# Kernel tuning notes

Measured on AMD Instinct MI355X. Metric: run time of the kernel, lower is better.

The kernel has to match this reference:

```python
import jax, jax.numpy as jnp
import numpy as np

B, S, I, Q, H = 512, 196, 2048, 1024, 512


def _attn(X, g, wx, bx, wg, bg, wh, bh):
    # X: (B, S, F); g: (B, G) or None
    feat = jnp.einsum('bsf,fh->bsh', X, wx) + bx
    if g is not None:
        feat = feat + (g @ wg + bg)[:, None, :]
    h = jnp.tanh(feat)
    score = jnp.einsum('bsh,h->bs', h, wh) + bh  # (B, S)
    a = jax.nn.softmax(score, axis=1)
    return jnp.einsum('bs,bsf->bf', a, X)


def setup_inputs() -> dict:
    key = jax.random.key(0)
    ks = jax.random.split(key, 16)
    sc = lambda n: 1.0 / np.sqrt(n)
    d = {
        'ques_feat': jax.random.normal(ks[0], (B, Q), jnp.float32),
        'img_feat': jax.random.normal(ks[1], (B, S, I), jnp.float32),
        # attn1: X=ques (Q), no guidance
        'w1x': jax.random.uniform(ks[2], (Q, H), jnp.float32, -sc(Q), sc(Q)),
        'b1x': jnp.zeros((H,), jnp.float32),
        'w1h': jax.random.uniform(ks[3], (H,), jnp.float32, -sc(H), sc(H)),
        'b1h': jnp.zeros((), jnp.float32),
        # attn2: X=img (I), guidance=ques (Q)
        'w2x': jax.random.uniform(ks[4], (I, H), jnp.float32, -sc(I), sc(I)),
        'b2x': jnp.zeros((H,), jnp.float32),
        'w2g': jax.random.uniform(ks[5], (Q, H), jnp.float32, -sc(Q), sc(Q)),
        'b2g': jnp.zeros((H,), jnp.float32),
        'w2h': jax.random.uniform(ks[6], (H,), jnp.float32, -sc(H), sc(H)),
        'b2h': jnp.zeros((), jnp.float32),
        # attn3: X=ques (Q), guidance=img-attended (I)
        'w3x': jax.random.uniform(ks[7], (Q, H), jnp.float32, -sc(Q), sc(Q)),
        'b3x': jnp.zeros((H,), jnp.float32),
        'w3g': jax.random.uniform(ks[8], (I, H), jnp.float32, -sc(I), sc(I)),
        'b3g': jnp.zeros((H,), jnp.float32),
        'w3h': jax.random.uniform(ks[9], (H,), jnp.float32, -sc(H), sc(H)),
        'b3h': jnp.zeros((), jnp.float32),
    }
    return d


def reference(ques_feat, img_feat, w1x, b1x, w1h, b1h, w2x, b2x, w2g, b2g,
              w2h, b2h, w3x, b3x, w3g, b3g, w3h, b3h):
    q = ques_feat[:, None, :]  # (B, 1, Q)
    ques_self = _attn(q, None, w1x, b1x, None, None, w1h, b1h)          # (B, Q)
    img_attn = _attn(img_feat, ques_self, w2x, b2x, w2g, b2g, w2h, b2h)  # (B, I)
    ques_attn = _attn(q, img_attn, w3x, b3x, w3g, b3g, w3h, b3h)         # (B, Q)
    return (ques_attn, img_attn)
```

## Files before the change

### kernel.cpp

```cpp
#include <hip/hip_runtime.h>
#include <hip/hip_bf16.h>
#include <cstdint>


typedef __attribute__((ext_vector_type(8))) short bf16x8;
typedef __attribute__((ext_vector_type(4))) float f32x4;

__device__ inline unsigned short f2bf(float f) {
    union { float f; unsigned u; } v; v.f = f;
    unsigned u = v.u;
    u += 0x7FFFu + ((u >> 16) & 1u);
    return (unsigned short)(u >> 16);
}

__device__ inline unsigned pk2(float lo, float hi) {
    __hip_bfloat162 h = __float22bfloat162_rn(make_float2(lo, hi));
    return *reinterpret_cast<unsigned*>(&h);
}

__global__ void k_copy(const float* __restrict__ src, float* __restrict__ dst) {
    int i = blockIdx.x * blockDim.x + threadIdx.x;
    reinterpret_cast<float4*>(dst)[i] = reinterpret_cast<const float4*>(src)[i];
}

__global__ void k_pack_w(const float* __restrict__ w, unsigned short* __restrict__ wtf) {
    int kblk = blockIdx.x >> 5;
    int nblk = blockIdx.x & 31;
    int t = threadIdx.x;
    int kc8 = t >> 4, col = t & 15;
    const float* src = w + (size_t)(kblk * 64 + kc8 * 8) * 512 + nblk * 16 + col;
    unsigned short* dst = wtf + (size_t)(kblk * 32 + nblk) * 1024 + kc8 * 128 + col * 8;
    unsigned short tmp[8];
    #pragma unroll
    for (int j = 0; j < 8; ++j) tmp[j] = f2bf(src[(size_t)j * 512]);
    *reinterpret_cast<uint4*>(dst) = *reinterpret_cast<const uint4*>(tmp);
}

__global__ void k_cconst(const float* __restrict__ qf, const float* __restrict__ w2g,
                         const float* __restrict__ b2g, const float* __restrict__ b2x,
                         float* __restrict__ cc) {
    __shared__ float qls[2][1024];
    int b0 = blockIdx.x * 2;
    int t = threadIdx.x;
    #pragma unroll
    for (int j = 0; j < 2; ++j) {
        int idx = j * 256 + t;
        int bb = idx >> 8, c4 = idx & 255;
        float4 v = reinterpret_cast<const float4*>(qf + (size_t)(b0 + bb) * 1024)[c4];
        qls[bb][c4 * 4 + 0] = v.x; qls[bb][c4 * 4 + 1] = v.y;
        qls[bb][c4 * 4 + 2] = v.z; qls[bb][c4 * 4 + 3] = v.w;
    }
    __syncthreads();
    float a00 = 0.f, a01 = 0.f, a10 = 0.f, a11 = 0.f;
    #pragma unroll 8
    for (int q = 0; q < 1024; ++q) {
        float w0 = w2g[q * 512 + t];
        float w1 = w2g[q * 512 + 256 + t];
        float q0 = qls[0][q], q1 = qls[1][q];
        a00 += q0 * w0; a01 += q0 * w1;
        a10 += q1 * w0; a11 += q1 * w1;
    }
    float c0 = b2g[t] + b2x[t];
    float c1 = b2g[t + 256] + b2x[t + 256];
    cc[(size_t)b0 * 512 + t] = a00 + c0;
    cc[(size_t)b0 * 512 + t + 256] = a01 + c1;
    cc[(size_t)(b0 + 1) * 512 + t] = a10 + c0;
    cc[(size_t)(b0 + 1) * 512 + t + 256] = a11 + c1;
}

#define NSTEP 32
struct ScoresCtx {
    const float* Xb; const unsigned short* WTf;
    unsigned short (*A)[112 * 64];
    int tid, wave, l15, l4;
};

__device__ __forceinline__ void sc_xload(const ScoresCtx& c, int t, float4 xv[2][2]) {
    int k0 = t * 64;
    #pragma unroll
    for (int u = 0; u < 2; ++u) {
        int id = c.tid + u * 512;
        if (id < 784) {
            int row = id >> 3, cc8 = id & 7;
            const float* p = c.Xb + (size_t)row * 2048 + k0 + cc8 * 8;
            xv[u][0] = *reinterpret_cast<const float4*>(p);
            xv[u][1] = *reinterpret_cast<const float4*>(p + 4);
        }
    }
}

__device__ __forceinline__ void sc_stagewrite(const ScoresCtx& c, int t, float4 xv[2][2]) {
    int buf = t & 1;
    #pragma unroll
    for (int u = 0; u < 2; ++u) {
        int id = c.tid + u * 512;
        if (id < 784) {
            int row = id >> 3, cc8 = id & 7;
            uint4 o;
            o.x = pk2(xv[u][0].x, xv[u][0].y);
            o.y = pk2(xv[u][0].z, xv[u][0].w);
            o.z = pk2(xv[u][1].x, xv[u][1].y);
            o.w = pk2(xv[u][1].z, xv[u][1].w);
            int idx = row * 64 + ((((cc8 * 16) ^ ((row & 7) << 4))) >> 1);
            *reinterpret_cast<uint4*>(&c.A[buf][idx]) = o;
        }
    }
}

__device__ __forceinline__ void sc_bload(const ScoresCtx& c, int t, bf16x8 br[8]) {
    const unsigned short* base = c.WTf + (size_t)t * 32768 + (size_t)c.wave * 4096;
    #pragma unroll
    for (int kh = 0; kh < 2; ++kh)
        #pragma unroll
        for (int n = 0; n < 4; ++n)
            br[kh * 4 + n] = *reinterpret_cast<const bf16x8*>(
                base + n * 1024 + (kh * 4 + c.l4) * 128 + c.l15 * 8);
}

__device__ __forceinline__ void sc_compute(const ScoresCtx& c, int t, bf16x8 br[8],
                                           f32x4 acc[7][4]) {
    int buf = t & 1;
    #pragma unroll
    for (int kh = 0; kh < 2; ++kh) {
        #pragma unroll
        for (int m = 0; m < 7; ++m) {
            int row = m * 16 + c.l15;
            int bofs = (kh * 64 + c.l4 * 16) ^ ((c.l15 & 7) << 4);
            bf16x8 af = *reinterpret_cast<const bf16x8*>(&c.A[buf][row * 64 + (bofs >> 1)]);
            #pragma unroll
            for (int n = 0; n < 4; ++n)
                acc[m][n] = __builtin_amdgcn_mfma_f32_16x16x32_bf16(af, br[kh * 4 + n],
                                                                    acc[m][n], 0, 0, 0);
        }
    }
}

__global__ __launch_bounds__(512, 2) void k_scores(
    const float* __restrict__ X, const unsigned short* __restrict__ WTf,
    const float* __restrict__ cc, const float* __restrict__ w2h,
    float* __restrict__ scores)
{
    __shared__ __align__(16) unsigned short A[2][112 * 64];
    __shared__ float slds[112];

    int bx = blockIdx.x;
    int b = bx >> 1;
    int s0 = (bx & 1) * 98;
    int tid = threadIdx.x;
    int wave = tid >> 6, lane = tid & 63;
    int l15 = lane & 15, l4 = lane >> 4;

    ScoresCtx c;
    c.Xb = X + (size_t)(b * 196 + s0) * 2048;
    c.WTf = WTf; c.A = A;
    c.tid = tid; c.wave = wave; c.l15 = l15; c.l4 = l4;

    float cch[4], whv[4];
    #pragma unroll
    for (int n = 0; n < 4; ++n) {
        int h = wave * 64 + n * 16 + l15;
        cch[n] = cc[(size_t)b * 512 + h];
        whv[n] = w2h[h];
    }

    for (int i = tid; i < 14 * 64; i += 512) { A[0][98 * 64 + i] = 0; A[1][98 * 64 + i] = 0; }
    if (tid < 112) slds[tid] = 0.0f;

    f32x4 acc[7][4];
    #pragma unroll
    for (int m = 0; m < 7; ++m)
        #pragma unroll
        for (int n = 0; n < 4; ++n) acc[m][n] = (f32x4){0.f, 0.f, 0.f, 0.f};

    float4 xvA[2][2], xvB[2][2];
    bf16x8 br[8];

    sc_xload(c, 0, xvA);
    sc_xload(c, 1, xvB);
    sc_stagewrite(c, 0, xvA);
    __syncthreads();

    #pragma unroll 1
    for (int t2 = 0; t2 < NSTEP; t2 += 2) {
        if (t2 + 2 < NSTEP) sc_xload(c, t2 + 2, xvA);
        sc_bload(c, t2, br);
        sc_compute(c, t2, br, acc);
        sc_stagewrite(c, t2 + 1, xvB);
        __syncthreads();
        if (t2 + 3 < NSTEP) sc_xload(c, t2 + 3, xvB);
        sc_bload(c, t2 + 1, br);
        sc_compute(c, t2 + 1, br, acc);
        if (t2 + 2 < NSTEP) sc_stagewrite(c, t2 + 2, xvA);
        __syncthreads();
    }

    #pragma unroll
    for (int m = 0; m < 7; ++m) {
        #pragma unroll
        for (int i = 0; i < 4; ++i) {
            float p = 0.0f;
            #pragma unroll
            for (int n = 0; n < 4; ++n) {
                float x = acc[m][n][i] + cch[n];
                float th = 1.0f - 2.0f / (__expf(2.0f * x) + 1.0f);
                p += th * whv[n];
            }
            p += __shfl_xor(p, 1);
            p += __shfl_xor(p, 2);
            p += __shfl_xor(p, 4);
            p += __shfl_xor(p, 8);
            if (l15 == 0) atomicAdd(&slds[m * 16 + l4 * 4 + i], p);
        }
    }
    __syncthreads();
    if (tid < 98) scores[(size_t)b * 208 + s0 + tid] = slds[tid];
}

__global__ void k_softmax(float* sc) {
    int b = blockIdx.x, t = threadIdx.x;
    __shared__ float red[8];
    float v = (t < 196) ? sc[(size_t)b * 208 + t] : -3.0e38f;
    float m = v;
    for (int o = 32; o > 0; o >>= 1) m = fmaxf(m, __shfl_xor(m, o));
    if ((t & 63) == 0) red[t >> 6] = m;
    __syncthreads();
    m = fmaxf(fmaxf(red[0], red[1]), fmaxf(red[2], red[3]));
    float e = (t < 196) ? __expf(v - m) : 0.0f;
    float s = e;
    for (int o = 32; o > 0; o >>= 1) s += __shfl_xor(s, o);
    if ((t & 63) == 0) red[4 + (t >> 6)] = s;
    __syncthreads();
    float tot = red[4] + red[5] + red[6] + red[7];
    if (t < 196) sc[(size_t)b * 208 + t] = e / tot;
}

__global__ void k_wsum(const float* __restrict__ X, const float* __restrict__ a,
                       float* __restrict__ out1) {
    __shared__ float als[196];
    int b = blockIdx.x >> 1;
    int fh = (blockIdx.x & 1) * 1024;
    int t = threadIdx.x;
    if (t < 196) als[t] = a[(size_t)b * 208 + t];
    __syncthreads();
    int f = fh + t * 4;
    const float* Xb = X + (size_t)b * 196 * 2048 + f;
    float4 acc = {0.f, 0.f, 0.f, 0.f};
    #pragma unroll 4
    for (int s = 0; s < 196; ++s) {
        float4 x = *reinterpret_cast<const float4*>(Xb + (size_t)s * 2048);
        float w = als[s];
        acc.x += w * x.x; acc.y += w * x.y; acc.z += w * x.z; acc.w += w * x.w;
    }
    *reinterpret_cast<float4*>(out1 + (size_t)b * 2048 + f) = acc;
}

extern "C" void kernel_launch(void* const* d_in, const int* in_sizes, int n_in,
                              void* d_out, int out_size, void* d_ws, size_t ws_size,
                              hipStream_t stream) {
    const float* qf  = (const float*)d_in[0];
    const float* X   = (const float*)d_in[1];
    const float* w2x = (const float*)d_in[6];
    const float* b2x = (const float*)d_in[7];
    const float* w2g = (const float*)d_in[8];
    const float* b2g = (const float*)d_in[9];
    const float* w2h = (const float*)d_in[10];

    float* out0 = (float*)d_out;
    float* out1 = out0 + 512 * 1024;

    unsigned short* WTf = (unsigned short*)d_ws;
    float* cc = (float*)((char*)d_ws + (size_t)(2u << 20));
    float* sc = (float*)((char*)d_ws + (size_t)(3u << 20));

    k_copy<<<512, 256, 0, stream>>>(qf, out0);
    k_pack_w<<<1024, 128, 0, stream>>>(w2x, WTf);
    k_cconst<<<256, 256, 0, stream>>>(qf, w2g, b2g, b2x, cc);
    k_scores<<<1024, 512, 0, stream>>>(X, WTf, cc, w2h, sc);
    k_softmax<<<512, 256, 0, stream>>>(sc);
    k_wsum<<<1024, 256, 0, stream>>>(X, sc, out1);
}
```

Measured before the change: 586.9 us.

## Tile scores GEMM over flattened rows in 64-row blocks spanning batch boundaries

The scores kernel now treats X as a flat (B*S, 2048) matrix and processes 64-row tiles (1568 blocks) rather than 98-row half-batches padded to 112. This removes the wasted MFMA work on padding rows, shrinks the accumulator and LDS footprint so launch bounds can request 4 blocks per CU, and adds s_setprio around the MFMA bursts. Tiles that straddle two batches choose the per-row guidance constant by comparing against the batch break. The score buffer stride changes from 208 to 196 to match.

```diff
diff --git a/kernel.cpp b/kernel.cpp
--- a/kernel.cpp
+++ b/kernel.cpp
@@ -69,139 +69,104 @@
 }
 
 #define NSTEP 32
-struct ScoresCtx {
-    const float* Xb; const unsigned short* WTf;
-    unsigned short (*A)[112 * 64];
-    int tid, wave, l15, l4;
-};
-
-__device__ __forceinline__ void sc_xload(const ScoresCtx& c, int t, float4 xv[2][2]) {
-    int k0 = t * 64;
-    #pragma unroll
-    for (int u = 0; u < 2; ++u) {
-        int id = c.tid + u * 512;
-        if (id < 784) {
-            int row = id >> 3, cc8 = id & 7;
-            const float* p = c.Xb + (size_t)row * 2048 + k0 + cc8 * 8;
-            xv[u][0] = *reinterpret_cast<const float4*>(p);
-            xv[u][1] = *reinterpret_cast<const float4*>(p + 4);
-        }
-    }
-}
-
-__device__ __forceinline__ void sc_stagewrite(const ScoresCtx& c, int t, float4 xv[2][2]) {
-    int buf = t & 1;
-    #pragma unroll
-    for (int u = 0; u < 2; ++u) {
-        int id = c.tid + u * 512;
-        if (id < 784) {
-            int row = id >> 3, cc8 = id & 7;
-            uint4 o;
-            o.x = pk2(xv[u][0].x, xv[u][0].y);
-            o.y = pk2(xv[u][0].z, xv[u][0].w);
-            o.z = pk2(xv[u][1].x, xv[u][1].y);
-            o.w = pk2(xv[u][1].z, xv[u][1].w);
-            int idx = row * 64 + ((((cc8 * 16) ^ ((row & 7) << 4))) >> 1);
-            *reinterpret_cast<uint4*>(&c.A[buf][idx]) = o;
-        }
-    }
-}
-
-__device__ __forceinline__ void sc_bload(const ScoresCtx& c, int t, bf16x8 br[8]) {
-    const unsigned short* base = c.WTf + (size_t)t * 32768 + (size_t)c.wave * 4096;
-    #pragma unroll
-    for (int kh = 0; kh < 2; ++kh)
-        #pragma unroll
-        for (int n = 0; n < 4; ++n)
-            br[kh * 4 + n] = *reinterpret_cast<const bf16x8*>(
-                base + n * 1024 + (kh * 4 + c.l4) * 128 + c.l15 * 8);
-}
-
-__device__ __forceinline__ void sc_compute(const ScoresCtx& c, int t, bf16x8 br[8],
-                                           f32x4 acc[7][4]) {
-    int buf = t & 1;
-    #pragma unroll
-    for (int kh = 0; kh < 2; ++kh) {
-        #pragma unroll
-        for (int m = 0; m < 7; ++m) {
-            int row = m * 16 + c.l15;
-            int bofs = (kh * 64 + c.l4 * 16) ^ ((c.l15 & 7) << 4);
-            bf16x8 af = *reinterpret_cast<const bf16x8*>(&c.A[buf][row * 64 + (bofs >> 1)]);
-            #pragma unroll
-            for (int n = 0; n < 4; ++n)
-                acc[m][n] = __builtin_amdgcn_mfma_f32_16x16x32_bf16(af, br[kh * 4 + n],
-                                                                    acc[m][n], 0, 0, 0);
-        }
-    }
-}
-
-__global__ __launch_bounds__(512, 2) void k_scores(
+
+__global__ __launch_bounds__(512, 4) void k_scores(
     const float* __restrict__ X, const unsigned short* __restrict__ WTf,
     const float* __restrict__ cc, const float* __restrict__ w2h,
     float* __restrict__ scores)
 {
-    __shared__ __align__(16) unsigned short A[2][112 * 64];
-    __shared__ float slds[112];
-
-    int bx = blockIdx.x;
-    int b = bx >> 1;
-    int s0 = (bx & 1) * 98;
+    __shared__ __align__(16) unsigned short A[2][64 * 64];
+    __shared__ float slds[64];
+
+    int tile = blockIdx.x;
     int tid = threadIdx.x;
     int wave = tid >> 6, lane = tid & 63;
     int l15 = lane & 15, l4 = lane >> 4;
 
-    ScoresCtx c;
-    c.Xb = X + (size_t)(b * 196 + s0) * 2048;
-    c.WTf = WTf; c.A = A;
-    c.tid = tid; c.wave = wave; c.l15 = l15; c.l4 = l4;
-
-    float cch[4], whv[4];
+    int r0 = tile * 64;
+    int b0 = r0 / 196;
+    int sbreak = (b0 + 1) * 196 - r0;
+    int b1 = b0 + 1; if (b1 > 511) b1 = 511;
+
+    int srow = tid >> 3, sc8 = tid & 7;
+    const float* xsrc = X + (size_t)(r0 + srow) * 2048 + sc8 * 8;
+    int sbyte = srow * 128 + ((sc8 * 16) ^ ((srow & 7) << 4));
+
+    float cch0[4], cch1[4], whv[4];
     #pragma unroll
     for (int n = 0; n < 4; ++n) {
         int h = wave * 64 + n * 16 + l15;
-        cch[n] = cc[(size_t)b * 512 + h];
+        cch0[n] = cc[(size_t)b0 * 512 + h];
+        cch1[n] = cc[(size_t)b1 * 512 + h];
         whv[n] = w2h[h];
     }
 
-    for (int i = tid; i < 14 * 64; i += 512) { A[0][98 * 64 + i] = 0; A[1][98 * 64 + i] = 0; }
-    if (tid < 112) slds[tid] = 0.0f;
-
-    f32x4 acc[7][4];
-    #pragma unroll
-    for (int m = 0; m < 7; ++m)
+    if (tid < 64) slds[tid] = 0.0f;
+
+    f32x4 acc[4][4];
+    #pragma unroll
+    for (int m = 0; m < 4; ++m)
         #pragma unroll
         for (int n = 0; n < 4; ++n) acc[m][n] = (f32x4){0.f, 0.f, 0.f, 0.f};
 
-    float4 xvA[2][2], xvB[2][2];
-    bf16x8 br[8];
-
-    sc_xload(c, 0, xvA);
-    sc_xload(c, 1, xvB);
-    sc_stagewrite(c, 0, xvA);
+    float4 xa0, xa1, xb0, xb1;
+
+    #define XLOAD(dst0, dst1, t) do { \
+        dst0 = *reinterpret_cast<const float4*>(xsrc + (t) * 64); \
+        dst1 = *reinterpret_cast<const float4*>(xsrc + (t) * 64 + 4); } while (0)
+
+    #define STAGE(t, v0, v1) do { \
+        uint4 o; \
+        o.x = pk2(v0.x, v0.y); o.y = pk2(v0.z, v0.w); \
+        o.z = pk2(v1.x, v1.y); o.w = pk2(v1.z, v1.w); \
+        *reinterpret_cast<uint4*>(reinterpret_cast<char*>(A[(t) & 1]) + sbyte) = o; } while (0)
+
+    #define COMPUTE(t) do { \
+        const unsigned short* base = WTf + (size_t)(t) * 32768 + (size_t)wave * 4096; \
+        _Pragma("unroll") \
+        for (int kh = 0; kh < 2; ++kh) { \
+            bf16x8 br[4]; \
+            _Pragma("unroll") \
+            for (int n = 0; n < 4; ++n) \
+                br[n] = *reinterpret_cast<const bf16x8*>(base + n * 1024 + (kh * 4 + l4) * 128 + l15 * 8); \
+            __builtin_amdgcn_s_setprio(1); \
+            _Pragma("unroll") \
+            for (int m = 0; m < 4; ++m) { \
+                int abyte = (m * 16 + l15) * 128 + (((kh * 64 + l4 * 16)) ^ ((l15 & 7) << 4)); \
+                bf16x8 af = *reinterpret_cast<const bf16x8*>( \
+                    reinterpret_cast<const char*>(A[(t) & 1]) + abyte); \
+                _Pragma("unroll") \
+                for (int n = 0; n < 4; ++n) \
+                    acc[m][n] = __builtin_amdgcn_mfma_f32_16x16x32_bf16(af, br[n], acc[m][n], 0, 0, 0); \
+            } \
+            __builtin_amdgcn_s_setprio(0); \
+        } } while (0)
+
+    XLOAD(xa0, xa1, 0);
+    XLOAD(xb0, xb1, 1);
+    STAGE(0, xa0, xa1);
     __syncthreads();
 
     #pragma unroll 1
     for (int t2 = 0; t2 < NSTEP; t2 += 2) {
-        if (t2 + 2 < NSTEP) sc_xload(c, t2 + 2, xvA);
-        sc_bload(c, t2, br);
-        sc_compute(c, t2, br, acc);
-        sc_stagewrite(c, t2 + 1, xvB);
+        if (t2 + 2 < NSTEP) XLOAD(xa0, xa1, t2 + 2);
+        COMPUTE(t2);
+        STAGE(t2 + 1, xb0, xb1);
         __syncthreads();
-        if (t2 + 3 < NSTEP) sc_xload(c, t2 + 3, xvB);
-        sc_bload(c, t2 + 1, br);
-        sc_compute(c, t2 + 1, br, acc);
-        if (t2 + 2 < NSTEP) sc_stagewrite(c, t2 + 2, xvA);
-        __syncthreads();
-    }
-
-    #pragma unroll
-    for (int m = 0; m < 7; ++m) {
+        if (t2 + 3 < NSTEP) XLOAD(xb0, xb1, t2 + 3);
+        COMPUTE(t2 + 1);
+        if (t2 + 2 < NSTEP) { STAGE(t2 + 2, xa0, xa1); __syncthreads(); }
+    }
+
+    #pragma unroll
+    for (int m = 0; m < 4; ++m) {
         #pragma unroll
         for (int i = 0; i < 4; ++i) {
+            int row = m * 16 + l4 * 4 + i;
             float p = 0.0f;
             #pragma unroll
             for (int n = 0; n < 4; ++n) {
-                float x = acc[m][n][i] + cch[n];
+                float x = acc[m][n][i] + ((row < sbreak) ? cch0[n] : cch1[n]);
                 float th = 1.0f - 2.0f / (__expf(2.0f * x) + 1.0f);
                 p += th * whv[n];
             }
@@ -209,17 +174,17 @@
             p += __shfl_xor(p, 2);
             p += __shfl_xor(p, 4);
             p += __shfl_xor(p, 8);
-            if (l15 == 0) atomicAdd(&slds[m * 16 + l4 * 4 + i], p);
+            if (l15 == 0) atomicAdd(&slds[row], p);
         }
     }
     __syncthreads();
-    if (tid < 98) scores[(size_t)b * 208 + s0 + tid] = slds[tid];
+    if (tid < 64) scores[(size_t)r0 + tid] = slds[tid];
 }
 
 __global__ void k_softmax(float* sc) {
     int b = blockIdx.x, t = threadIdx.x;
     __shared__ float red[8];
-    float v = (t < 196) ? sc[(size_t)b * 208 + t] : -3.0e38f;
+    float v = (t < 196) ? sc[(size_t)b * 196 + t] : -3.0e38f;
     float m = v;
     for (int o = 32; o > 0; o >>= 1) m = fmaxf(m, __shfl_xor(m, o));
     if ((t & 63) == 0) red[t >> 6] = m;
@@ -231,7 +196,7 @@
     if ((t & 63) == 0) red[4 + (t >> 6)] = s;
     __syncthreads();
     float tot = red[4] + red[5] + red[6] + red[7];
-    if (t < 196) sc[(size_t)b * 208 + t] = e / tot;
+    if (t < 196) sc[(size_t)b * 196 + t] = e / tot;
 }
 
 __global__ void k_wsum(const float* __restrict__ X, const float* __restrict__ a,
@@ -240,7 +205,7 @@
     int b = blockIdx.x >> 1;
     int fh = (blockIdx.x & 1) * 1024;
     int t = threadIdx.x;
-    if (t < 196) als[t] = a[(size_t)b * 208 + t];
+    if (t < 196) als[t] = a[(size_t)b * 196 + t];
     __syncthreads();
     int f = fh + t * 4;
     const float* Xb = X + (size_t)b * 196 * 2048 + f;
@@ -275,7 +240,7 @@
     k_copy<<<512, 256, 0, stream>>>(qf, out0);
     k_pack_w<<<1024, 128, 0, stream>>>(w2x, WTf);
     k_cconst<<<256, 256, 0, stream>>>(qf, w2g, b2g, b2x, cc);
-    k_scores<<<1024, 512, 0, stream>>>(X, WTf, cc, w2h, sc);
+    k_scores<<<1568, 512, 0, stream>>>(X, WTf, cc, w2h, sc);
     k_softmax<<<512, 256, 0, stream>>>(sc);
     k_wsum<<<1024, 256, 0, stream>>>(X, sc, out1);
 }
```

Result: slower. 789.1 us (+34.5%).
